# Performance work log

Measured on AMD Instinct MI355X. Metric: run time of the kernel, lower is better.

The kernel has to match this reference:

```python
import jax, jax.numpy as jnp
import numpy as np

POS = np.array([[0,3,0.5],[0,3,1.5],[0,3,2.5],[0,3,3.5],[0,3,4.5],[0,3,5.5],[1,0,0],[1,6,6],[2,0,6],[2,6,0],[3,0,0],[3,6,6],[4,0,6],[4,6,0],[5,0,0],[5,6,6],[6,0,6],[6,6,0],[7,0,0],[7,6,6],[8,0,6],[8,6,0],[9,0,0],[9,6,6],[10,0,6],[10,6,0],[11,0,0],[11,6,6],[12,0,6],[12,6,0],[13,0,0],[13,6,6],[14,0,6],[14,6,0],[15,0,0],[15,6,6],[16,0,6],[16,6,0],[17,0.5,0.5],[17,3,0.5],[17,5.5,0.5],[17,0.5,3],[17,3,3],[17,5.5,3],[17,0.5,5.5],[17,3,5.5],[17,5.5,5.5]], dtype=np.float32)  # (47,3) fixed buffer

B, S, D, H, FF, HID = 512, 47, 32, 4, 2048, 256

def _ln(x, w, b, eps=1e-5):
    mu = jnp.mean(x, -1, keepdims=True)
    var = jnp.mean((x - mu) ** 2, -1, keepdims=True)
    return (x - mu) * jax.lax.rsqrt(var + eps) * w + b

def _encoder_layer(h, wi, bi, wo, bo, l1w, l1b, f1w, f1b, f2w, f2b, l2w, l2b):
    # torch post-norm TransformerEncoderLayer; batch_first=False => attention over axis 0
    L, N, E = h.shape
    Dh = E // H
    qkv = h @ wi.T + bi                                  # (L,N,3E)
    q, k, v = jnp.split(qkv, 3, axis=-1)
    q = q.reshape(L, N, H, Dh); k = k.reshape(L, N, H, Dh); v = v.reshape(L, N, H, Dh)
    scores = jnp.einsum('lnhd,mnhd->nhlm', q, k) * (1.0 / np.sqrt(Dh))  # (N,H,L,L)
    a = jax.nn.softmax(scores, axis=-1)
    o = jnp.einsum('nhlm,mnhd->lnhd', a, v).reshape(L, N, E)
    h = _ln(h + (o @ wo.T + bo), l1w, l1b)
    ff = jax.nn.relu(h @ f1w.T + f1b) @ f2w.T + f2b
    return _ln(h + ff, l2w, l2b)

def setup_inputs():
    key = jax.random.key(0)
    ks = list(jax.random.split(key, 24))
    rn = lambda k, s, sc=0.05: jax.random.normal(k, s, jnp.float32) * sc
    return dict(
        x=jax.random.normal(ks[0], (B, S), jnp.float32),
        w_in=rn(ks[1], (D, 1)), b_in=rn(ks[2], (D,)),
        w_pos=rn(ks[3], (D, 3)), b_pos=rn(ks[4], (D,)),
        cls_token=rn(ks[5], (1, 1, D), 1.0),
        attn_in_w=rn(ks[6], (2, 3 * D, D)), attn_in_b=rn(ks[7], (2, 3 * D)),
        attn_out_w=rn(ks[8], (2, D, D)), attn_out_b=rn(ks[9], (2, D)),
        ln1_w=jnp.ones((2, D)), ln1_b=jnp.zeros((2, D)),
        ff1_w=rn(ks[10], (2, FF, D)), ff1_b=rn(ks[11], (2, FF)),
        ff2_w=rn(ks[12], (2, D, FF)), ff2_b=rn(ks[13], (2, D)),
        ln2_w=jnp.ones((2, D)), ln2_b=jnp.zeros((2, D)),
        out_w=rn(ks[14], (1, D)), out_b=rn(ks[15], (1,)),
        mlp_w0=rn(ks[16], (HID, S)), mlp_b0=rn(ks[17], (HID,)),
        mlp_w1=rn(ks[18], (HID, HID)), mlp_b1=rn(ks[19], (HID,)),
        mlp_w2=rn(ks[20], (1, HID)), mlp_b2=rn(ks[21], (1,)),
    )

def reference(x, w_in, b_in, w_pos, b_pos, cls_token, attn_in_w, attn_in_b, attn_out_w, attn_out_b, ln1_w, ln1_b, ff1_w, ff1_b, ff2_w, ff2_b, ln2_w, ln2_b, out_w, out_b, mlp_w0, mlp_b0, mlp_w1, mlp_b1, mlp_w2, mlp_b2):
    Bn = x.shape[0]
    h = x[..., None] * w_in[:, 0] + b_in                 # Linear(1,D): (B,S,D)
    h = h + (jnp.asarray(POS) @ w_pos.T + b_pos)         # pos projection (S,D)
    cls = jnp.broadcast_to(cls_token, (Bn, 1, D))
    h = jnp.concatenate([cls, h], axis=1)                # (B,S+1,D)
    for i in range(2):
        h = _encoder_layer(h, attn_in_w[i], attn_in_b[i], attn_out_w[i], attn_out_b[i], ln1_w[i], ln1_b[i], ff1_w[i], ff1_b[i], ff2_w[i], ff2_b[i], ln2_w[i], ln2_b[i])
    out = jax.nn.relu(h[:, 1:, :] @ out_w.T + out_b)[..., 0]   # (B,S); dropout = eval identity
    o = jax.nn.relu(out @ mlp_w0.T + mlp_b0)
    o = jax.nn.relu(o @ mlp_w1.T + mlp_b1)
    o = jax.nn.relu(o @ mlp_w2.T + mlp_b2)               # MLP ends with ReLU per source
    return o
```

## Files before the change

### kernel.cpp

```cpp
#include <hip/hip_runtime.h>

#define NB 512
#define NS 47
#define NP 48
#define DIM 32
#define NFF 2048
#define NHID 256
#define NROWS (NB * NP)
#define FTOK 96

#define VSTR 520
#define PSTR 72
#define USTR 136

typedef _Float16 f16x8 __attribute__((ext_vector_type(8)));
typedef _Float16 f16x4 __attribute__((ext_vector_type(4)));
typedef float f32x4 __attribute__((ext_vector_type(4)));

__constant__ float POSC[NS * 3] = {
  0,3,0.5f, 0,3,1.5f, 0,3,2.5f, 0,3,3.5f, 0,3,4.5f, 0,3,5.5f,
  1,0,0, 1,6,6, 2,0,6, 2,6,0, 3,0,0, 3,6,6, 4,0,6, 4,6,0,
  5,0,0, 5,6,6, 6,0,6, 6,6,0, 7,0,0, 7,6,6, 8,0,6, 8,6,0,
  9,0,0, 9,6,6, 10,0,6, 10,6,0, 11,0,0, 11,6,6, 12,0,6, 12,6,0,
  13,0,0, 13,6,6, 14,0,6, 14,6,0, 15,0,0, 15,6,6, 16,0,6, 16,6,0,
  17,0.5f,0.5f, 17,3,0.5f, 17,5.5f,0.5f, 17,0.5f,3, 17,3,3, 17,5.5f,3,
  17,0.5f,5.5f, 17,3,5.5f, 17,5.5f,5.5f
};

__global__ __launch_bounds__(256) void prep_embed_kernel(
    const float* __restrict__ w1, const float* __restrict__ w2,
    _Float16* __restrict__ w1h, _Float16* __restrict__ w2h,
    const float* __restrict__ x, const float* __restrict__ w_in,
    const float* __restrict__ b_in, const float* __restrict__ w_pos,
    const float* __restrict__ b_pos, const float* __restrict__ cls,
    float* __restrict__ h) {
  const int bx = blockIdx.x;
  if (bx < 512) {
    int idx = bx * 256 + threadIdx.x;
    w1h[idx] = (_Float16)w1[idx];
    w2h[idx] = (_Float16)w2[idx];
    return;
  }
  int idx = (bx - 512) * 256 + threadIdx.x;
  int r = idx >> 5, d = idx & 31;
  int l = r / NP, n = r - l * NP;
  float v;
  if (n == 0) {
    v = cls[d];
  } else {
    int s = n - 1;
    v = x[l * NS + s] * w_in[d] + b_in[d]
      + POSC[s * 3 + 0] * w_pos[d * 3 + 0]
      + POSC[s * 3 + 1] * w_pos[d * 3 + 1]
      + POSC[s * 3 + 2] * w_pos[d * 3 + 2] + b_pos[d];
  }
  h[idx] = v;
}

__global__ __launch_bounds__(256) void kv_kernel(
    const float* __restrict__ h, const float* __restrict__ wi, const float* __restrict__ bi,
    _Float16* __restrict__ Kp, _Float16* __restrict__ Vt) {
  __shared__ float ws_[512];
  __shared__ float bs_[16];
  const int t = threadIdx.x;
  const int nh = blockIdx.x >> 1;
  const int n = nh >> 2, hh = nh & 3;
  const int l = ((blockIdx.x & 1) << 8) | t;
  for (int i = t; i < 512; i += 256) {
    int sub = i >> 8, rem = i & 255;
    int jj = rem >> 5, d = rem & 31;
    ws_[i] = wi[((sub + 1) * 32 + hh * 8 + jj) * 32 + d];
  }
  if (t < 16) bs_[t] = bi[((t >> 3) + 1) * 32 + hh * 8 + (t & 7)];
  __syncthreads();
  const float4* hrow = (const float4*)(h + (l * NP + n) * 32);
  float4 hv[8];
  #pragma unroll
  for (int i = 0; i < 8; ++i) hv[i] = hrow[i];
  f16x8 kh, kl_, vh;
  #pragma unroll
  for (int jj = 0; jj < 8; ++jj) {
    float k0 = bs_[jj], k1 = 0.f, k2 = 0.f, k3 = 0.f;
    float v0 = bs_[8 + jj], v1 = 0.f, v2 = 0.f, v3 = 0.f;
    #pragma unroll
    for (int d4 = 0; d4 < 8; ++d4) {
      float4 hvv = hv[d4];
      k0 += hvv.x * ws_[jj * 32 + 4 * d4 + 0];
      k1 += hvv.y * ws_[jj * 32 + 4 * d4 + 1];
      k2 += hvv.z * ws_[jj * 32 + 4 * d4 + 2];
      k3 += hvv.w * ws_[jj * 32 + 4 * d4 + 3];
      v0 += hvv.x * ws_[256 + jj * 32 + 4 * d4 + 0];
      v1 += hvv.y * ws_[256 + jj * 32 + 4 * d4 + 1];
      v2 += hvv.z * ws_[256 + jj * 32 + 4 * d4 + 2];
      v3 += hvv.w * ws_[256 + jj * 32 + 4 * d4 + 3];
    }
    float kv = (k0 + k1) + (k2 + k3);
    float vv = (v0 + v1) + (v2 + v3);
    kh[jj] = (_Float16)kv; kl_[jj] = (_Float16)(kv - (float)kh[jj]);
    vh[jj] = (_Float16)vv;
  }
  _Float16* kdst = Kp + ((size_t)nh * 512 + l) * 16;
  *(f16x8*)(kdst) = kh;
  *(f16x8*)(kdst + 8) = kl_;
  #pragma unroll
  for (int d = 0; d < 8; ++d) Vt[(size_t)nh * 4096 + d * 512 + l] = vh[d];
}

__global__ __launch_bounds__(256, 2) void attn_mfma_kernel(
    const float* __restrict__ h, const float* __restrict__ wi, const float* __restrict__ bi,
    const _Float16* __restrict__ Kp, const _Float16* __restrict__ Vt,
    float* __restrict__ o) {
  __shared__ alignas(16) _Float16 khi[512 * 8];
  __shared__ alignas(16) _Float16 klo[512 * 8];
  __shared__ alignas(16) _Float16 vts[8 * VSTR];
  __shared__ alignas(16) float hq_pls[4608];
  __shared__ alignas(16) _Float16 qf[128 * 16];
  __shared__ float wsq[256];
  __shared__ float bq[8];
  const int bx = blockIdx.x;
  const int nh = bx >> 2, qc = bx & 3;
  const int n = nh >> 2, hh = nh & 3;
  const int t = threadIdx.x;
  const int lane = t & 63, wv = t >> 6;
  const int c = lane & 15, g = lane >> 4;

  const _Float16* kg = Kp + (size_t)nh * 8192;
  for (int r = t; r < 512; r += 256) {
    const uint4* src = (const uint4*)(kg + r * 16);
    uint4 a = src[0], b = src[1];
    *(uint4*)(khi + r * 8) = a;
    *(uint4*)(klo + r * 8) = b;
  }
  {
    const _Float16* vg = Vt + (size_t)nh * 4096;
    for (int i = t; i < 512; i += 256) {
      int d = i >> 6, seg = i & 63;
      *(uint4*)(vts + d * VSTR + seg * 8) = *(const uint4*)(vg + d * 512 + seg * 8);
    }
  }
  wsq[t] = wi[(hh * 8 + (t & 7)) * 32 + (t >> 3)];
  if (t < 8) bq[t] = bi[hh * 8 + t];
  float* hq = hq_pls;

  #pragma unroll
  for (int rp = 0; rp < 2; ++rp) {
    {
      int row = t >> 2, quar = t & 3;
      const float4* src =
          (const float4*)(h + (((qc * 128 + rp * 64 + row) * NP) + n) * 32 + quar * 8);
      float4 a = src[0], b = src[1];
      __syncthreads();
      *(float4*)(hq + row * 36 + quar * 8) = a;
      *(float4*)(hq + row * 36 + quar * 8 + 4) = b;
    }
    __syncthreads();
    {
      int row = t >> 2, pr = t & 3;
      #pragma unroll
      for (int u = 0; u < 2; ++u) {
        int jj = pr * 2 + u;
        float a = bq[jj];
        #pragma unroll
        for (int d = 0; d < 32; ++d) a += hq[row * 36 + d] * wsq[d * 8 + jj];
        _Float16 qh = (_Float16)a;
        _Float16 ql = (_Float16)(a - (float)qh);
        qf[(rp * 64 + row) * 16 + jj] = qh;
        qf[(rp * 64 + row) * 16 + 8 + jj] = ql;
      }
    }
    __syncthreads();
  }

  const f16x8 hz = {(_Float16)0,(_Float16)0,(_Float16)0,(_Float16)0,
                    (_Float16)0,(_Float16)0,(_Float16)0,(_Float16)0};
  const f32x4 zf = {0.f, 0.f, 0.f, 0.f};
  _Float16* pls_ = (_Float16*)hq_pls;
  _Float16* mypA = pls_ + wv * (16 * PSTR);
  _Float16* mypB = pls_ + (4 + wv) * (16 * PSTR);
  const int q0A = qc * 128 + wv * 16;
  const int q0B = q0A + 64;

  f16x8 aqA = hz, aqB = hz;
  if (g < 3) {
    aqA = *(const f16x8*)(qf + (wv * 16 + c) * 16 + (g & 1) * 8);
    aqB = *(const f16x8*)(qf + (64 + wv * 16 + c) * 16 + (g & 1) * 8);
  }
  f32x4 accA = {0.f, 0.f, 0.f, 0.f}, accB = {0.f, 0.f, 0.f, 0.f};
  float lsA[4] = {0.f, 0.f, 0.f, 0.f}, lsB[4] = {0.f, 0.f, 0.f, 0.f};

  for (int ch = 0; ch < 8; ++ch) {
    const int kb = ch * 64;
    #pragma unroll
    for (int kt = 0; kt < 4; ++kt) {
      f16x8 bk = hz;
      if (g < 2)       bk = *(const f16x8*)(khi + (kb + kt * 16 + c) * 8);
      else if (g == 2) bk = *(const f16x8*)(klo + (kb + kt * 16 + c) * 8);
      f32x4 sA = __builtin_amdgcn_mfma_f32_16x16x32_f16(aqA, bk, zf, 0, 0, 0);
      f32x4 sB = __builtin_amdgcn_mfma_f32_16x16x32_f16(aqB, bk, zf, 0, 0, 0);
      #pragma unroll
      for (int r = 0; r < 4; ++r) {
        float pA = __expf(sA[r] * 0.35355339059327373f - 2.0f);
        float pB = __expf(sB[r] * 0.35355339059327373f - 2.0f);
        _Float16 phA = (_Float16)pA;
        _Float16 phB = (_Float16)pB;
        lsA[r] += (float)phA;
        lsB[r] += (float)phB;
        mypA[(g * 4 + r) * PSTR + kt * 16 + c] = phA;
        mypB[(g * 4 + r) * PSTR + kt * 16 + c] = phB;
      }
    }
    #pragma unroll
    for (int half = 0; half < 2; ++half) {
      f16x8 bv = hz;
      if (c < 8) bv = *(const f16x8*)(vts + c * VSTR + kb + half * 32 + g * 8);
      f16x8 apA = *(const f16x8*)(mypA + c * PSTR + half * 32 + g * 8);
      f16x8 apB = *(const f16x8*)(mypB + c * PSTR + half * 32 + g * 8);
      accA = __builtin_amdgcn_mfma_f32_16x16x32_f16(apA, bv, accA, 0, 0, 0);
      accB = __builtin_amdgcn_mfma_f32_16x16x32_f16(apB, bv, accB, 0, 0, 0);
    }
  }
  #pragma unroll
  for (int m = 1; m < 16; m <<= 1) {
    #pragma unroll
    for (int r = 0; r < 4; ++r) {
      lsA[r] += __shfl_xor(lsA[r], m, 64);
      lsB[r] += __shfl_xor(lsB[r], m, 64);
    }
  }
  if (c < 8) {
    #pragma unroll
    for (int r = 0; r < 4; ++r) {
      o[((q0A + g * 4 + r) * NP + n) * 32 + hh * 8 + c] = accA[r] / lsA[r];
      o[((q0B + g * 4 + r) * NP + n) * 32 + hh * 8 + c] = accB[r] / lsB[r];
    }
  }
}

__global__ __launch_bounds__(256) void proj_ln1_kernel(
    const float* __restrict__ o, const float* __restrict__ wo, const float* __restrict__ bo,
    const float* __restrict__ lw, const float* __restrict__ lb, float* __restrict__ h) {
  __shared__ float wos[32 * 33];
  __shared__ float pre[64 * 33];
  const int g = blockIdx.x, t = threadIdx.x;
  for (int i = t; i < 1024; i += 256) wos[(i >> 5) * 33 + (i & 31)] = wo[i];
  __syncthreads();
  const int subr = t >> 2, jq = t & 3;
  const int r = g * 64 + subr;
  const float4* orow = (const float4*)(o + r * 32);
  float4 ov[8];
  #pragma unroll
  for (int i = 0; i < 8; ++i) ov[i] = orow[i];
  const float* hres = h + r * 32 + jq * 8;
  #pragma unroll
  for (int jj = 0; jj < 8; ++jj) {
    int j = jq * 8 + jj;
    float a0 = bo[j], a1 = 0.f, a2 = 0.f, a3 = 0.f;
    #pragma unroll
    for (int d4 = 0; d4 < 8; ++d4) {
      float4 vv = ov[d4];
      a0 += vv.x * wos[j * 33 + 4 * d4 + 0];
      a1 += vv.y * wos[j * 33 + 4 * d4 + 1];
      a2 += vv.z * wos[j * 33 + 4 * d4 + 2];
      a3 += vv.w * wos[j * 33 + 4 * d4 + 3];
    }
    pre[subr * 33 + j] = (a0 + a1) + (a2 + a3) + hres[jj];
  }
  __syncthreads();
  if (t < 64) {
    float mu = 0.f;
    #pragma unroll
    for (int d = 0; d < 32; ++d) mu += pre[t * 33 + d];
    mu *= (1.f / 32.f);
    float var = 0.f;
    #pragma unroll
    for (int d = 0; d < 32; ++d) { float dv = pre[t * 33 + d] - mu; var += dv * dv; }
    float rs = rsqrtf(var * (1.f / 32.f) + 1e-5f);
    float* hrow = h + (g * 64 + t) * 32;
    #pragma unroll
    for (int d = 0; d < 32; ++d)
      hrow[d] = (pre[t * 33 + d] - mu) * rs * lw[d] + lb[d];
  }
}

__global__ __launch_bounds__(256) void ff_fused_kernel(
    const float* __restrict__ h, const _Float16* __restrict__ w1h,
    const float* __restrict__ b1, const _Float16* __restrict__ w2h,
    const float* __restrict__ b2, const float* __restrict__ lw,
    const float* __restrict__ lb, const float* __restrict__ ow,
    const float* __restrict__ ob, float* __restrict__ svec, int do_svec) {
  __shared__ alignas(16) _Float16 ubuf[4][2][16 * USTR];
  __shared__ alignas(16) float yw[4][FTOK * 33];
  const int t = threadIdx.x;
  const int lane = t & 63;
  const int wv = t >> 6;
  const int nl = lane & 15;
  const int g = lane >> 4;
  const int g4 = g * 4;
  const int r0 = blockIdx.x * FTOK;

  f16x8 hfrag[6];
  #pragma unroll
  for (int tt = 0; tt < 6; ++tt) {
    const float4 h0 = *(const float4*)(h + (r0 + tt * 16 + nl) * 32 + g * 8);
    const float4 h1 = *(const float4*)(h + (r0 + tt * 16 + nl) * 32 + g * 8 + 4);
    hfrag[tt][0] = (_Float16)h0.x; hfrag[tt][1] = (_Float16)h0.y;
    hfrag[tt][2] = (_Float16)h0.z; hfrag[tt][3] = (_Float16)h0.w;
    hfrag[tt][4] = (_Float16)h1.x; hfrag[tt][5] = (_Float16)h1.y;
    hfrag[tt][6] = (_Float16)h1.z; hfrag[tt][7] = (_Float16)h1.w;
  }

  f32x4 acc0[6], acc1[6];
  #pragma unroll
  for (int tt = 0; tt < 6; ++tt) {
    acc0[tt] = (f32x4){0.f, 0.f, 0.f, 0.f};
    acc1[tt] = (f32x4){0.f, 0.f, 0.f, 0.f};
  }
  const f32x4 zero = {0.f, 0.f, 0.f, 0.f};
  const int ffbase = wv * 512;

  #pragma unroll
  for (int sc = 0; sc < 4; ++sc) {
    const int ffb = ffbase + sc * 128;
    f16x8 wf[8];
    float4 bv[8];
    #pragma unroll
    for (int ft = 0; ft < 8; ++ft) {
      wf[ft] = *(const f16x8*)(w1h + (ffb + ft * 16 + nl) * 32 + g * 8);
      bv[ft] = *(const float4*)(b1 + ffb + ft * 16 + g4);
    }
    f16x8 w2f0[4], w2f1[4];
    #pragma unroll
    for (int kk = 0; kk < 4; ++kk) {
      w2f0[kk] = *(const f16x8*)(w2h + nl * NFF + ffb + kk * 32 + g * 8);
      w2f1[kk] = *(const f16x8*)(w2h + (16 + nl) * NFF + ffb + kk * 32 + g * 8);
    }
    #pragma unroll
    for (int tt = 0; tt < 6; ++tt) {
      _Float16* ub = ubuf[wv][tt & 1];
      f32x4 cc[8];
      #pragma unroll
      for (int ft = 0; ft < 8; ++ft)
        cc[ft] = __builtin_amdgcn_mfma_f32_16x16x32_f16(wf[ft], hfrag[tt], zero, 0, 0, 0);
      #pragma unroll
      for (int ft = 0; ft < 8; ++ft) {
        f16x4 uv;
        uv[0] = (_Float16)fmaxf(cc[ft][0] + bv[ft].x, 0.f);
        uv[1] = (_Float16)fmaxf(cc[ft][1] + bv[ft].y, 0.f);
        uv[2] = (_Float16)fmaxf(cc[ft][2] + bv[ft].z, 0.f);
        uv[3] = (_Float16)fmaxf(cc[ft][3] + bv[ft].w, 0.f);
        *(f16x4*)(ub + nl * USTR + ft * 16 + g4) = uv;
      }
      #pragma unroll
      for (int kk = 0; kk < 4; ++kk) {
        f16x8 uf = *(const f16x8*)(ub + nl * USTR + kk * 32 + g * 8);
        acc0[tt] = __builtin_amdgcn_mfma_f32_16x16x32_f16(uf, w2f0[kk], acc0[tt], 0, 0, 0);
        acc1[tt] = __builtin_amdgcn_mfma_f32_16x16x32_f16(uf, w2f1[kk], acc1[tt], 0, 0, 0);
      }
    }
  }
  #pragma unroll
  for (int tt = 0; tt < 6; ++tt) {
    #pragma unroll
    for (int r = 0; r < 4; ++r) {
      yw[wv][(tt * 16 + g4 + r) * 33 + nl]      = acc0[tt][r];
      yw[wv][(tt * 16 + g4 + r) * 33 + 16 + nl] = acc1[tt][r];
    }
  }
  __syncthreads();

  float* pre = (float*)ubuf;
  {
    int idx = t;
    #pragma unroll
    for (int u = 0; u < 12; ++u, idx += 256) {
      int tok = idx >> 5, d = idx & 31;
      int off = tok * 33 + d;
      float v = yw[0][off] + yw[1][off] + yw[2][off] + yw[3][off]
              + b2[d] + h[(r0 + tok) * 32 + d];
      pre[off] = v;
    }
  }
  __syncthreads();

  if (t < FTOK) {
    float mu = 0.f;
    #pragma unroll
    for (int d = 0; d < 32; ++d) mu += pre[t * 33 + d];
    mu *= (1.f / 32.f);
    float var = 0.f;
    #pragma unroll
    for (int d = 0; d < 32; ++d) { float dv = pre[t * 33 + d] - mu; var += dv * dv; }
    float rs = rsqrtf(var * (1.f / 32.f) + 1e-5f);
    const int rr = r0 + t;
    float* hrow = (float*)h + (size_t)rr * 32;
    float hn[32];
    #pragma unroll
    for (int d = 0; d < 32; ++d) {
      hn[d] = (pre[t * 33 + d] - mu) * rs * lw[d] + lb[d];
      hrow[d] = hn[d];
    }
    if (do_svec) {
      int l = rr / NP, n = rr - l * NP;
      if (n > 0) {
        float a = ob[0];
        #pragma unroll
        for (int d = 0; d < 32; ++d) a += hn[d] * ow[d];
        svec[l * NS + (n - 1)] = fmaxf(a, 0.f);
      }
    }
  }
}

__global__ __launch_bounds__(256) void head_kernel(
    const float* __restrict__ svec,
    const float* __restrict__ m0w, const float* __restrict__ m0b,
    const float* __restrict__ m1w, const float* __restrict__ m1b,
    const float* __restrict__ m2w, const float* __restrict__ m2b,
    float* __restrict__ out) {
  __shared__ float sv[NS];
  __shared__ float hid[NHID];
  __shared__ float red[4];
  const int l = blockIdx.x, t = threadIdx.x;
  if (t < NS) sv[t] = svec[l * NS + t];
  __syncthreads();
  {
    float a = m0b[t];
    const float* wr = m0w + t * NS;
    #pragma unroll
    for (int s = 0; s < NS; ++s) a += sv[s] * wr[s];
    hid[t] = fmaxf(a, 0.f);
  }
  __syncthreads();
  {
    float a = m1b[t];
    const float4* wr = (const float4*)(m1w + t * NHID);
    #pragma unroll 8
    for (int j4 = 0; j4 < 64; ++j4) {
      float4 w = wr[j4];
      a += hid[4 * j4 + 0] * w.x + hid[4 * j4 + 1] * w.y
         + hid[4 * j4 + 2] * w.z + hid[4 * j4 + 3] * w.w;
    }
    float h2 = fmaxf(a, 0.f);
    float part = h2 * m2w[t];
    #pragma unroll
    for (int off = 32; off > 0; off >>= 1) part += __shfl_down(part, off, 64);
    if ((t & 63) == 0) red[t >> 6] = part;
  }
  __syncthreads();
  if (t == 0) out[l] = fmaxf(red[0] + red[1] + red[2] + red[3] + m2b[0], 0.f);
}

extern "C" void kernel_launch(void* const* d_in, const int* in_sizes, int n_in,
                              void* d_out, int out_size, void* d_ws, size_t ws_size,
                              hipStream_t stream) {
  (void)in_sizes; (void)n_in; (void)out_size; (void)ws_size;
  const float* x     = (const float*)d_in[0];
  const float* w_in  = (const float*)d_in[1];
  const float* b_in  = (const float*)d_in[2];
  const float* w_pos = (const float*)d_in[3];
  const float* b_pos = (const float*)d_in[4];
  const float* cls   = (const float*)d_in[5];
  const float* wi    = (const float*)d_in[6];
  const float* bi    = (const float*)d_in[7];
  const float* wo    = (const float*)d_in[8];
  const float* bo    = (const float*)d_in[9];
  const float* l1w   = (const float*)d_in[10];
  const float* l1b   = (const float*)d_in[11];
  const float* f1w   = (const float*)d_in[12];
  const float* f1b   = (const float*)d_in[13];
  const float* f2w   = (const float*)d_in[14];
  const float* f2b   = (const float*)d_in[15];
  const float* l2w   = (const float*)d_in[16];
  const float* l2b   = (const float*)d_in[17];
  const float* ow    = (const float*)d_in[18];
  const float* ob    = (const float*)d_in[19];
  const float* m0w   = (const float*)d_in[20];
  const float* m0b   = (const float*)d_in[21];
  const float* m1w   = (const float*)d_in[22];
  const float* m1b   = (const float*)d_in[23];
  const float* m2w   = (const float*)d_in[24];
  const float* m2b   = (const float*)d_in[25];
  float* out = (float*)d_out;

  float* ws   = (float*)d_ws;
  float* h    = ws;
  float* o    = ws + 786432;
  float* R2   = ws + 1572864;
  _Float16* Kp = (_Float16*)R2;
  _Float16* Vt = (_Float16*)(R2 + 786432);
  float* svec = ws + 2752512;
  _Float16* w1h = (_Float16*)(ws + 2776576);
  _Float16* w2h = (_Float16*)(ws + 2842112);

  prep_embed_kernel<<<3584, 256, 0, stream>>>(f1w, f2w, w1h, w2h,
                                              x, w_in, b_in, w_pos, b_pos, cls, h);
  for (int L = 0; L < 2; ++L) {
    kv_kernel<<<384, 256, 0, stream>>>(h, wi + L * 3072, bi + L * 96, Kp, Vt);
    attn_mfma_kernel<<<768, 256, 0, stream>>>(h, wi + L * 3072, bi + L * 96, Kp, Vt, o);
    proj_ln1_kernel<<<384, 256, 0, stream>>>(o, wo + L * 1024, bo + L * 32,
                                             l1w + L * 32, l1b + L * 32, h);
    ff_fused_kernel<<<256, 256, 0, stream>>>(h, w1h + L * 65536, f1b + L * NFF,
                                             w2h + L * 65536, f2b + L * 32,
                                             l2w + L * 32, l2b + L * 32,
                                             ow, ob, svec, L);
  }
  head_kernel<<<512, 256, 0, stream>>>(svec, m0w, m0b, m1w, m1b, m2w, m2b, out);
}
```

Baseline: 154.9 us.

## Restructure FF kernel to stream FF-chunk weights through LDS per token tile

The fused FFN kernel now gives each wave its own 16-token tile and has all four waves walk the full 2048-wide hidden dimension together. 64-wide weight chunks are staged in shared memory with register prefetch of the next chunk, and the cross-wave partial-sum reduction is removed. W2 is pre-permuted in the prep kernel into a chunk-contiguous layout, and the token tile shrinks from 96 to 64, so the grid grows to 384 blocks. The attention kernel's occupancy hint also rises from 2 to 3. The FFN change adds two block barriers per chunk (64 per block) and leaves less register-level reuse of the weights.

```diff
diff --git a/kernel.cpp b/kernel.cpp
--- a/kernel.cpp
+++ b/kernel.cpp
@@ -7,11 +7,11 @@
 #define NFF 2048
 #define NHID 256
 #define NROWS (NB * NP)
-#define FTOK 96
+#define FTOK 64
 
 #define VSTR 520
 #define PSTR 72
-#define USTR 136
+#define USTR 72
 
 typedef _Float16 f16x8 __attribute__((ext_vector_type(8)));
 typedef _Float16 f16x4 __attribute__((ext_vector_type(4)));
@@ -38,7 +38,9 @@
   if (bx < 512) {
     int idx = bx * 256 + threadIdx.x;
     w1h[idx] = (_Float16)w1[idx];
-    w2h[idx] = (_Float16)w2[idx];
+    int l = idx >> 16, r = idx & 65535, d = r >> 11, ff = r & 2047;
+    int dst = ((l * 64 + (ff >> 5)) * 32 + d) * 32 + (ff & 31);
+    w2h[dst] = (_Float16)w2[idx];
     return;
   }
   int idx = (bx - 512) * 256 + threadIdx.x;
@@ -106,7 +108,7 @@
   for (int d = 0; d < 8; ++d) Vt[(size_t)nh * 4096 + d * 512 + l] = vh[d];
 }
 
-__global__ __launch_bounds__(256, 2) void attn_mfma_kernel(
+__global__ __launch_bounds__(256, 3) void attn_mfma_kernel(
     const float* __restrict__ h, const float* __restrict__ wi, const float* __restrict__ bi,
     const _Float16* __restrict__ Kp, const _Float16* __restrict__ Vt,
     float* __restrict__ o) {
@@ -288,8 +290,11 @@
     const float* __restrict__ b2, const float* __restrict__ lw,
     const float* __restrict__ lb, const float* __restrict__ ow,
     const float* __restrict__ ob, float* __restrict__ svec, int do_svec) {
-  __shared__ alignas(16) _Float16 ubuf[4][2][16 * USTR];
-  __shared__ alignas(16) float yw[4][FTOK * 33];
+  __shared__ alignas(16) _Float16 wlds1[2048];
+  __shared__ alignas(16) _Float16 wlds2[2048];
+  __shared__ alignas(16) float bias_lds[2048];
+  __shared__ alignas(16) _Float16 ubuf[4][16 * USTR];
+  __shared__ alignas(16) float pre_s[64 * 33];
   const int t = threadIdx.x;
   const int lane = t & 63;
   const int wv = t >> 6;
@@ -297,106 +302,103 @@
   const int g = lane >> 4;
   const int g4 = g * 4;
   const int r0 = blockIdx.x * FTOK;
-
-  f16x8 hfrag[6];
-  #pragma unroll
-  for (int tt = 0; tt < 6; ++tt) {
-    const float4 h0 = *(const float4*)(h + (r0 + tt * 16 + nl) * 32 + g * 8);
-    const float4 h1 = *(const float4*)(h + (r0 + tt * 16 + nl) * 32 + g * 8 + 4);
-    hfrag[tt][0] = (_Float16)h0.x; hfrag[tt][1] = (_Float16)h0.y;
-    hfrag[tt][2] = (_Float16)h0.z; hfrag[tt][3] = (_Float16)h0.w;
-    hfrag[tt][4] = (_Float16)h1.x; hfrag[tt][5] = (_Float16)h1.y;
-    hfrag[tt][6] = (_Float16)h1.z; hfrag[tt][7] = (_Float16)h1.w;
-  }
-
-  f32x4 acc0[6], acc1[6];
-  #pragma unroll
-  for (int tt = 0; tt < 6; ++tt) {
-    acc0[tt] = (f32x4){0.f, 0.f, 0.f, 0.f};
-    acc1[tt] = (f32x4){0.f, 0.f, 0.f, 0.f};
-  }
+  _Float16* ub = ubuf[wv];
+
+  {
+    const float4* bsrc = (const float4*)b1;
+    float4 ba = bsrc[t * 2], bb = bsrc[t * 2 + 1];
+    *(float4*)(bias_lds + t * 8) = ba;
+    *(float4*)(bias_lds + t * 8 + 4) = bb;
+  }
+  f16x8 hfrag;
+  {
+    const float4 h0 = *(const float4*)(h + (r0 + wv * 16 + nl) * 32 + g * 8);
+    const float4 h1 = *(const float4*)(h + (r0 + wv * 16 + nl) * 32 + g * 8 + 4);
+    hfrag[0] = (_Float16)h0.x; hfrag[1] = (_Float16)h0.y;
+    hfrag[2] = (_Float16)h0.z; hfrag[3] = (_Float16)h0.w;
+    hfrag[4] = (_Float16)h1.x; hfrag[5] = (_Float16)h1.y;
+    hfrag[6] = (_Float16)h1.z; hfrag[7] = (_Float16)h1.w;
+  }
+  {
+    uint4 c1 = ((const uint4*)w1h)[t];
+    uint4 c2 = ((const uint4*)w2h)[t];
+    ((uint4*)wlds1)[t] = c1;
+    ((uint4*)wlds2)[t] = c2;
+  }
+  __syncthreads();
+
+  f32x4 acc0 = {0.f, 0.f, 0.f, 0.f};
+  f32x4 acc1 = {0.f, 0.f, 0.f, 0.f};
   const f32x4 zero = {0.f, 0.f, 0.f, 0.f};
-  const int ffbase = wv * 512;
-
-  #pragma unroll
-  for (int sc = 0; sc < 4; ++sc) {
-    const int ffb = ffbase + sc * 128;
-    f16x8 wf[8];
-    float4 bv[8];
-    #pragma unroll
-    for (int ft = 0; ft < 8; ++ft) {
-      wf[ft] = *(const f16x8*)(w1h + (ffb + ft * 16 + nl) * 32 + g * 8);
-      bv[ft] = *(const float4*)(b1 + ffb + ft * 16 + g4);
-    }
-    f16x8 w2f0[4], w2f1[4];
-    #pragma unroll
-    for (int kk = 0; kk < 4; ++kk) {
-      w2f0[kk] = *(const f16x8*)(w2h + nl * NFF + ffb + kk * 32 + g * 8);
-      w2f1[kk] = *(const f16x8*)(w2h + (16 + nl) * NFF + ffb + kk * 32 + g * 8);
-    }
-    #pragma unroll
-    for (int tt = 0; tt < 6; ++tt) {
-      _Float16* ub = ubuf[wv][tt & 1];
-      f32x4 cc[8];
-      #pragma unroll
-      for (int ft = 0; ft < 8; ++ft)
-        cc[ft] = __builtin_amdgcn_mfma_f32_16x16x32_f16(wf[ft], hfrag[tt], zero, 0, 0, 0);
-      #pragma unroll
-      for (int ft = 0; ft < 8; ++ft) {
-        f16x4 uv;
-        uv[0] = (_Float16)fmaxf(cc[ft][0] + bv[ft].x, 0.f);
-        uv[1] = (_Float16)fmaxf(cc[ft][1] + bv[ft].y, 0.f);
-        uv[2] = (_Float16)fmaxf(cc[ft][2] + bv[ft].z, 0.f);
-        uv[3] = (_Float16)fmaxf(cc[ft][3] + bv[ft].w, 0.f);
-        *(f16x4*)(ub + nl * USTR + ft * 16 + g4) = uv;
-      }
-      #pragma unroll
-      for (int kk = 0; kk < 4; ++kk) {
-        f16x8 uf = *(const f16x8*)(ub + nl * USTR + kk * 32 + g * 8);
-        acc0[tt] = __builtin_amdgcn_mfma_f32_16x16x32_f16(uf, w2f0[kk], acc0[tt], 0, 0, 0);
-        acc1[tt] = __builtin_amdgcn_mfma_f32_16x16x32_f16(uf, w2f1[kk], acc1[tt], 0, 0, 0);
-      }
-    }
-  }
-  #pragma unroll
-  for (int tt = 0; tt < 6; ++tt) {
-    #pragma unroll
-    for (int r = 0; r < 4; ++r) {
-      yw[wv][(tt * 16 + g4 + r) * 33 + nl]      = acc0[tt][r];
-      yw[wv][(tt * 16 + g4 + r) * 33 + 16 + nl] = acc1[tt][r];
-    }
-  }
-  __syncthreads();
-
-  float* pre = (float*)ubuf;
-  {
-    int idx = t;
-    #pragma unroll
-    for (int u = 0; u < 12; ++u, idx += 256) {
-      int tok = idx >> 5, d = idx & 31;
-      int off = tok * 33 + d;
-      float v = yw[0][off] + yw[1][off] + yw[2][off] + yw[3][off]
-              + b2[d] + h[(r0 + tok) * 32 + d];
-      pre[off] = v;
-    }
+
+  for (int sc = 0; sc < 32; ++sc) {
+    uint4 n1, n2;
+    if (sc + 1 < 32) {
+      n1 = ((const uint4*)(w1h + (sc + 1) * 2048))[t];
+      n2 = ((const uint4*)(w2h + (sc + 1) * 2048))[t];
+    }
+    f16x8 wf[4];
+    float4 bv[4];
+    #pragma unroll
+    for (int ft = 0; ft < 4; ++ft) {
+      wf[ft] = *(const f16x8*)(wlds1 + (ft * 16 + nl) * 32 + g * 8);
+      bv[ft] = *(const float4*)(bias_lds + sc * 64 + ft * 16 + g4);
+    }
+    f32x4 cc[4];
+    #pragma unroll
+    for (int ft = 0; ft < 4; ++ft)
+      cc[ft] = __builtin_amdgcn_mfma_f32_16x16x32_f16(wf[ft], hfrag, zero, 0, 0, 0);
+    #pragma unroll
+    for (int ft = 0; ft < 4; ++ft) {
+      f16x4 uv;
+      uv[0] = (_Float16)fmaxf(cc[ft][0] + bv[ft].x, 0.f);
+      uv[1] = (_Float16)fmaxf(cc[ft][1] + bv[ft].y, 0.f);
+      uv[2] = (_Float16)fmaxf(cc[ft][2] + bv[ft].z, 0.f);
+      uv[3] = (_Float16)fmaxf(cc[ft][3] + bv[ft].w, 0.f);
+      *(f16x4*)(ub + nl * USTR + ft * 16 + g4) = uv;
+    }
+    #pragma unroll
+    for (int kk = 0; kk < 2; ++kk) {
+      f16x8 uf = *(const f16x8*)(ub + nl * USTR + kk * 32 + g * 8);
+      f16x8 wa = *(const f16x8*)(wlds2 + kk * 1024 + nl * 32 + g * 8);
+      f16x8 wb = *(const f16x8*)(wlds2 + kk * 1024 + (16 + nl) * 32 + g * 8);
+      acc0 = __builtin_amdgcn_mfma_f32_16x16x32_f16(uf, wa, acc0, 0, 0, 0);
+      acc1 = __builtin_amdgcn_mfma_f32_16x16x32_f16(uf, wb, acc1, 0, 0, 0);
+    }
+    __syncthreads();
+    if (sc + 1 < 32) {
+      ((uint4*)wlds1)[t] = n1;
+      ((uint4*)wlds2)[t] = n2;
+    }
+    __syncthreads();
+  }
+
+  #pragma unroll
+  for (int r = 0; r < 4; ++r) {
+    pre_s[(wv * 16 + g4 + r) * 33 + nl]      = acc0[r];
+    pre_s[(wv * 16 + g4 + r) * 33 + 16 + nl] = acc1[r];
   }
   __syncthreads();
 
   if (t < FTOK) {
+    const int rr = r0 + t;
+    const float* hres = h + (size_t)rr * 32;
+    float pv[32];
+    #pragma unroll
+    for (int d = 0; d < 32; ++d) pv[d] = pre_s[t * 33 + d] + b2[d] + hres[d];
     float mu = 0.f;
     #pragma unroll
-    for (int d = 0; d < 32; ++d) mu += pre[t * 33 + d];
+    for (int d = 0; d < 32; ++d) mu += pv[d];
     mu *= (1.f / 32.f);
     float var = 0.f;
     #pragma unroll
-    for (int d = 0; d < 32; ++d) { float dv = pre[t * 33 + d] - mu; var += dv * dv; }
+    for (int d = 0; d < 32; ++d) { float dv = pv[d] - mu; var += dv * dv; }
     float rs = rsqrtf(var * (1.f / 32.f) + 1e-5f);
-    const int rr = r0 + t;
     float* hrow = (float*)h + (size_t)rr * 32;
     float hn[32];
     #pragma unroll
     for (int d = 0; d < 32; ++d) {
-      hn[d] = (pre[t * 33 + d] - mu) * rs * lw[d] + lb[d];
+      hn[d] = (pv[d] - mu) * rs * lw[d] + lb[d];
       hrow[d] = hn[d];
     }
     if (do_svec) {
@@ -499,7 +501,7 @@
     attn_mfma_kernel<<<768, 256, 0, stream>>>(h, wi + L * 3072, bi + L * 96, Kp, Vt, o);
     proj_ln1_kernel<<<384, 256, 0, stream>>>(o, wo + L * 1024, bo + L * 32,
                                              l1w + L * 32, l1b + L * 32, h);
-    ff_fused_kernel<<<256, 256, 0, stream>>>(h, w1h + L * 65536, f1b + L * NFF,
+    ff_fused_kernel<<<384, 256, 0, stream>>>(h, w1h + L * 65536, f1b + L * NFF,
                                              w2h + L * 65536, f2b + L * 32,
                                              l2w + L * 32, l2b + L * 32,
                                              ow, ob, svec, L);
```

Result: slower. 164.0 us (+5.9%).
